# Kernel optimization log

Hardware: AMD Instinct MI355X
Metric: run time of the kernel (lower is better)

The kernel has to match this reference:

```python
import jax, jax.numpy as jnp
import numpy as np

N_NODE = 50000
D_FEAT = 128
N_EDGE = 625000
SIM_THRESH = 0.1


def setup_inputs() -> dict:
    key = jax.random.key(0)
    k1, k2, k3, k4, k5 = jax.random.split(key, 5)
    features = jax.random.normal(k1, (N_NODE, D_FEAT), dtype=jnp.float32)
    edge_weight = jax.random.uniform(k2, (N_EDGE,), dtype=jnp.float32)
    gate = jax.random.uniform(k3, (1,), dtype=jnp.float32)
    row = jax.random.randint(k4, (N_EDGE,), 0, N_NODE)
    col = jax.random.randint(k5, (N_EDGE,), 0, N_NODE)
    # avoid self-loops so the original's att[0,0]==0 / diagonal-removal branches
    # behave as the common (no self-loop) path
    col = jnp.where(col == row, (col + 1) % N_NODE, col)
    edge_index = jnp.stack([row, col], axis=0).astype(jnp.int64)
    return {"edge_index": edge_index, "edge_weight": edge_weight,
            "features": features, "gate": gate}


def reference(edge_index, edge_weight, features, gate):
    n_node = features.shape[0]
    row, col = edge_index[0], edge_index[1]
    # per-edge cosine similarity via normalized feature gather
    nrm = jnp.maximum(jnp.linalg.norm(features, axis=1, keepdims=True), 1e-12)
    fn = features / nrm
    sim = jnp.sum(fn[row] * fn[col], axis=1)            # [E]
    sim = jnp.where(sim < SIM_THRESH, 0.0, sim)         # threshold (all remaining >= 0.1)
    # row-wise L1 normalize over the sparse adjacency
    row_sum = jax.ops.segment_sum(jnp.abs(sim), row, num_segments=n_node)  # [N]
    denom = jnp.where(row_sum > 0, row_sum, 1.0)
    sim_norm = sim / denom[row]
    # degree-based self-loop weight lam = 1/(deg+1); only affects diagonal edges
    degree = jax.ops.segment_sum((sim_norm != 0).astype(sim_norm.dtype), row,
                                 num_segments=n_node)
    lam = 1.0 / (degree + 1.0)
    att_edge = sim_norm + jnp.where(row == col, lam[row], 0.0)
    att_edge = jnp.exp(att_edge)
    # learnable gate blend + clamp
    out = gate[0] * edge_weight + (1.0 - gate[0]) * att_edge
    return jnp.maximum(out, 0.0)
```

## Files before the change

### kernel.cpp

```cpp
#include <hip/hip_runtime.h>
#include <hip/hip_fp16.h>
#include <math.h>

#define N_NODE 50000
#define D_FEAT 128
#define N_EDGE 625000
#define SIM_THRESH 0.1f
#define BAND_EPS 1e-3f


__global__ void prep_kernel(const float* __restrict__ feat,
                            float* __restrict__ inv_nrm,
                            __half* __restrict__ fn16,
                            float* __restrict__ row_sum,
                            float* __restrict__ degree,
                            unsigned int* __restrict__ band_count) {
    int g = blockIdx.x * blockDim.x + threadIdx.x;
    if (g < N_NODE) { row_sum[g] = 0.0f; degree[g] = 0.0f; }
    if (g == 0) *band_count = 0u;
    int node = g >> 5;
    int lane = g & 31;
    if (node >= N_NODE) return;
    const float4* f = (const float4*)(feat + (size_t)node * D_FEAT);
    float4 v = f[lane];
    float ss = v.x * v.x + v.y * v.y + v.z * v.z + v.w * v.w;
#pragma unroll
    for (int o = 16; o > 0; o >>= 1)
        ss += __shfl_down(ss, o, 32);
    ss = __shfl(ss, 0, 32);
    float inv = 1.0f / fmaxf(sqrtf(ss), 1e-12f);
    if (lane == 0) inv_nrm[node] = inv;
    __half2 h0 = __floats2half2_rn(v.x * inv, v.y * inv);
    __half2 h1 = __floats2half2_rn(v.z * inv, v.w * inv);
    __half2* dst = (__half2*)(fn16 + (size_t)node * D_FEAT);
    dst[lane * 2]     = h0;
    dst[lane * 2 + 1] = h1;
}

__global__ void edge_sim16_kernel(const int* __restrict__ row,
                                  const int* __restrict__ col,
                                  const __half* __restrict__ fn16,
                                  float* __restrict__ sim_out,
                                  float* __restrict__ row_sum,
                                  float* __restrict__ degree,
                                  unsigned int* __restrict__ band_count,
                                  unsigned int* __restrict__ band_list) {
    int g = blockIdx.x * blockDim.x + threadIdx.x;
    int edge = g >> 4;
    int lane = g & 15;
    if (edge >= N_EDGE) return;
    int r = row[edge];
    int c = col[edge];
    float4 a = ((const float4*)(fn16 + (size_t)r * D_FEAT))[lane];
    float4 b = ((const float4*)(fn16 + (size_t)c * D_FEAT))[lane];
    const __half2* ah = (const __half2*)&a;
    const __half2* bh = (const __half2*)&b;
    float d = 0.0f;
#pragma unroll
    for (int i = 0; i < 4; i++) {
        float2 af = __half22float2(ah[i]);
        float2 bf = __half22float2(bh[i]);
        d = fmaf(af.x, bf.x, d);
        d = fmaf(af.y, bf.y, d);
    }
#pragma unroll
    for (int o = 8; o > 0; o >>= 1)
        d += __shfl_down(d, o, 16);
    if (lane == 0) {
        float s = d;
        if (fabsf(s - SIM_THRESH) < BAND_EPS) {
            unsigned int idx = atomicAdd(band_count, 1u);
            band_list[idx] = (unsigned int)edge;
        } else {
            if (s < SIM_THRESH) s = 0.0f;
            sim_out[edge] = s;
            if (s != 0.0f) {
                atomicAdd(&row_sum[r], s);
                atomicAdd(&degree[r], 1.0f);
            }
        }
    }
}

__global__ void band_fix_kernel(const int* __restrict__ row,
                                const int* __restrict__ col,
                                const float* __restrict__ feat,
                                const float* __restrict__ inv_nrm,
                                const unsigned int* __restrict__ band_count,
                                const unsigned int* __restrict__ band_list,
                                float* __restrict__ sim_out,
                                float* __restrict__ row_sum,
                                float* __restrict__ degree) {
    int g = blockIdx.x * blockDim.x + threadIdx.x;
    int group = g >> 5;
    int lane = g & 31;
    int ngroups = (gridDim.x * blockDim.x) >> 5;
    unsigned int cnt = *band_count;
    for (unsigned int i = group; i < cnt; i += ngroups) {
        int e = (int)band_list[i];
        int r = row[e], c = col[e];
        float4 a = ((const float4*)(feat + (size_t)r * D_FEAT))[lane];
        float4 b = ((const float4*)(feat + (size_t)c * D_FEAT))[lane];
        float d = a.x * b.x + a.y * b.y + a.z * b.z + a.w * b.w;
#pragma unroll
        for (int o = 16; o > 0; o >>= 1)
            d += __shfl_down(d, o, 32);
        if (lane == 0) {
            float s = d * inv_nrm[r] * inv_nrm[c];
            if (s < SIM_THRESH) s = 0.0f;
            sim_out[e] = s;
            if (s != 0.0f) {
                atomicAdd(&row_sum[r], s);
                atomicAdd(&degree[r], 1.0f);
            }
        }
    }
}

__global__ void edge_out_kernel(const int* __restrict__ row,
                                const int* __restrict__ col,
                                const float* __restrict__ sim,
                                const float* __restrict__ row_sum,
                                const float* __restrict__ degree,
                                const float* __restrict__ ew,
                                const float* __restrict__ gate,
                                float* __restrict__ out) {
    int e = blockIdx.x * blockDim.x + threadIdx.x;
    if (e >= N_EDGE) return;
    int r = row[e];
    float rs = row_sum[r];
    float denom = (rs > 0.0f) ? rs : 1.0f;
    float att = sim[e] / denom;
    if (r == col[e]) att += 1.0f / (degree[r] + 1.0f);
    att = expf(att);
    float gv = gate[0];
    float o = gv * ew[e] + (1.0f - gv) * att;
    out[e] = fmaxf(o, 0.0f);
}

__global__ void inv_norm_kernel(const float* __restrict__ feat,
                                float* __restrict__ inv_nrm) {
    int g = blockIdx.x * blockDim.x + threadIdx.x;
    int node = g >> 5;
    int lane = g & 31;
    if (node >= N_NODE) return;
    const float4* f = (const float4*)(feat + (size_t)node * D_FEAT);
    float4 v = f[lane];
    float ss = v.x * v.x + v.y * v.y + v.z * v.z + v.w * v.w;
#pragma unroll
    for (int o = 16; o > 0; o >>= 1)
        ss += __shfl_down(ss, o, 32);
    if (lane == 0) {
        float n = fmaxf(sqrtf(ss), 1e-12f);
        inv_nrm[node] = 1.0f / n;
    }
}

__global__ void edge_sim_kernel(const int* __restrict__ row,
                                const int* __restrict__ col,
                                const float* __restrict__ feat,
                                const float* __restrict__ inv_nrm,
                                float* __restrict__ sim_out,
                                float* __restrict__ row_sum,
                                float* __restrict__ degree) {
    int g = blockIdx.x * blockDim.x + threadIdx.x;
    int edge = g >> 5;
    int lane = g & 31;
    if (edge >= N_EDGE) return;
    int r = row[edge];
    int c = col[edge];
    float4 a = ((const float4*)(feat + (size_t)r * D_FEAT))[lane];
    float4 b = ((const float4*)(feat + (size_t)c * D_FEAT))[lane];
    float d = a.x * b.x + a.y * b.y + a.z * b.z + a.w * b.w;
#pragma unroll
    for (int o = 16; o > 0; o >>= 1)
        d += __shfl_down(d, o, 32);
    if (lane == 0) {
        float s = d * inv_nrm[r] * inv_nrm[c];
        if (s < SIM_THRESH) s = 0.0f;
        sim_out[edge] = s;
        if (s != 0.0f) {
            atomicAdd(&row_sum[r], s);
            atomicAdd(&degree[r], 1.0f);
        }
    }
}

extern "C" void kernel_launch(void* const* d_in, const int* in_sizes, int n_in,
                              void* d_out, int out_size, void* d_ws, size_t ws_size,
                              hipStream_t stream) {
    const int*   edge_index = (const int*)d_in[0];
    const float* ew         = (const float*)d_in[1];
    const float* feat       = (const float*)d_in[2];
    const float* gate       = (const float*)d_in[3];
    float*       out        = (float*)d_out;

    const int* row = edge_index;
    const int* col = edge_index + N_EDGE;

    float* row_sum = (float*)d_ws;
    float* degree  = row_sum + N_NODE;
    float* inv_nrm = degree + N_NODE;
    float* sim     = inv_nrm + N_NODE;
    __half* fn16   = (__half*)(sim + N_EDGE);
    unsigned int* band_list  = (unsigned int*)(fn16 + (size_t)N_NODE * D_FEAT);
    unsigned int* band_count = band_list + N_EDGE;

    size_t need = (size_t)(3 * N_NODE + N_EDGE) * 4
                + (size_t)N_NODE * D_FEAT * 2
                + (size_t)(N_EDGE + 1) * 4;

    const int block = 256;

    if (ws_size >= need) {
        {
            long long threads = (long long)N_NODE * 32;
            prep_kernel<<<(int)((threads + block - 1) / block), block, 0, stream>>>(
                feat, inv_nrm, fn16, row_sum, degree, band_count);
        }
        {
            long long threads = (long long)N_EDGE * 16;
            edge_sim16_kernel<<<(int)((threads + block - 1) / block), block, 0, stream>>>(
                row, col, fn16, sim, row_sum, degree, band_count, band_list);
        }
        band_fix_kernel<<<64, block, 0, stream>>>(
            row, col, feat, inv_nrm, band_count, band_list, sim, row_sum, degree);
        edge_out_kernel<<<(N_EDGE + block - 1) / block, block, 0, stream>>>(
            row, col, sim, row_sum, degree, ew, gate, out);
    } else {
        hipMemsetAsync(d_ws, 0, (size_t)2 * N_NODE * sizeof(float), stream);
        {
            long long threads = (long long)N_NODE * 32;
            inv_norm_kernel<<<(int)((threads + block - 1) / block), block, 0, stream>>>(
                feat, inv_nrm);
        }
        {
            long long threads = (long long)N_EDGE * 32;
            edge_sim_kernel<<<(int)((threads + block - 1) / block), block, 0, stream>>>(
                row, col, feat, inv_nrm, sim, row_sum, degree);
        }
        edge_out_kernel<<<(N_EDGE + block - 1) / block, block, 0, stream>>>(
            row, col, sim, row_sum, degree, ew, gate, out);
    }
}
```

Baseline: 149.5 us.

## Screen edges with fp8 dot product before fp16 and fp32 refinement

Adds an fp8 copy of the normalized features and computes a cheap fp8 dot product per edge first. Only edges whose fp8 similarity exceeds a screening bound (0.07) load fp16 features, and near-threshold edges fall back inline to fp32, which replaces the separate band list and band-fix kernel. This cuts gather traffic for the many edges far below the threshold and drops one kernel launch. The risk is that fp8 error could wrongly drop edges with true similarity just above 0.1, and the inline fp32 path adds divergence.

```diff
diff --git a/kernel.cpp b/kernel.cpp
--- a/kernel.cpp
+++ b/kernel.cpp
@@ -6,113 +6,112 @@
 #define D_FEAT 128
 #define N_EDGE 625000
 #define SIM_THRESH 0.1f
-#define BAND_EPS 1e-3f
-
+#define SCREEN_LO 0.07f
+#define BAND_EPS 5e-4f
+
+typedef float v2f __attribute__((ext_vector_type(2)));
 
 __global__ void prep_kernel(const float* __restrict__ feat,
                             float* __restrict__ inv_nrm,
                             __half* __restrict__ fn16,
+                            unsigned int* __restrict__ fp8tab,
                             float* __restrict__ row_sum,
-                            float* __restrict__ degree,
-                            unsigned int* __restrict__ band_count) {
+                            float* __restrict__ degree) {
     int g = blockIdx.x * blockDim.x + threadIdx.x;
     if (g < N_NODE) { row_sum[g] = 0.0f; degree[g] = 0.0f; }
-    if (g == 0) *band_count = 0u;
     int node = g >> 5;
     int lane = g & 31;
     if (node >= N_NODE) return;
-    const float4* f = (const float4*)(feat + (size_t)node * D_FEAT);
-    float4 v = f[lane];
+    float4 v = ((const float4*)(feat + (size_t)node * D_FEAT))[lane];
     float ss = v.x * v.x + v.y * v.y + v.z * v.z + v.w * v.w;
 #pragma unroll
-    for (int o = 16; o > 0; o >>= 1)
-        ss += __shfl_down(ss, o, 32);
+    for (int o = 16; o > 0; o >>= 1) ss += __shfl_down(ss, o, 32);
     ss = __shfl(ss, 0, 32);
     float inv = 1.0f / fmaxf(sqrtf(ss), 1e-12f);
     if (lane == 0) inv_nrm[node] = inv;
-    __half2 h0 = __floats2half2_rn(v.x * inv, v.y * inv);
-    __half2 h1 = __floats2half2_rn(v.z * inv, v.w * inv);
-    __half2* dst = (__half2*)(fn16 + (size_t)node * D_FEAT);
-    dst[lane * 2]     = h0;
-    dst[lane * 2 + 1] = h1;
-}
-
-__global__ void edge_sim16_kernel(const int* __restrict__ row,
-                                  const int* __restrict__ col,
-                                  const __half* __restrict__ fn16,
-                                  float* __restrict__ sim_out,
-                                  float* __restrict__ row_sum,
-                                  float* __restrict__ degree,
-                                  unsigned int* __restrict__ band_count,
-                                  unsigned int* __restrict__ band_list) {
+    float x0 = v.x * inv, x1 = v.y * inv, x2 = v.z * inv, x3 = v.w * inv;
+    __half2 h0 = __floats2half2_rn(x0, x1);
+    __half2 h1 = __floats2half2_rn(x2, x3);
+    uint2 p;
+    p.x = *(unsigned int*)&h0;
+    p.y = *(unsigned int*)&h1;
+    ((uint2*)(fn16 + (size_t)node * D_FEAT))[lane] = p;
+    int w = __builtin_amdgcn_cvt_pk_fp8_f32(x0, x1, 0, false);
+    w = __builtin_amdgcn_cvt_pk_fp8_f32(x2, x3, w, true);
+    fp8tab[(size_t)node * 32 + lane] = (unsigned int)w;
+}
+
+__global__ void edge_sim8_kernel(const int* __restrict__ row,
+                                 const int* __restrict__ col,
+                                 const float* __restrict__ feat,
+                                 const float* __restrict__ inv_nrm,
+                                 const __half* __restrict__ fn16,
+                                 const unsigned int* __restrict__ fp8tab,
+                                 float* __restrict__ sim_out,
+                                 float* __restrict__ row_sum,
+                                 float* __restrict__ degree) {
     int g = blockIdx.x * blockDim.x + threadIdx.x;
     int edge = g >> 4;
     int lane = g & 15;
     if (edge >= N_EDGE) return;
     int r = row[edge];
     int c = col[edge];
-    float4 a = ((const float4*)(fn16 + (size_t)r * D_FEAT))[lane];
-    float4 b = ((const float4*)(fn16 + (size_t)c * D_FEAT))[lane];
-    const __half2* ah = (const __half2*)&a;
-    const __half2* bh = (const __half2*)&b;
+
+    uint2 aw = ((const uint2*)(fp8tab + (size_t)r * 32))[lane];
+    uint2 bw = ((const uint2*)(fp8tab + (size_t)c * 32))[lane];
+    v2f a01 = __builtin_amdgcn_cvt_pk_f32_fp8((int)aw.x, false);
+    v2f a23 = __builtin_amdgcn_cvt_pk_f32_fp8((int)aw.x, true);
+    v2f a45 = __builtin_amdgcn_cvt_pk_f32_fp8((int)aw.y, false);
+    v2f a67 = __builtin_amdgcn_cvt_pk_f32_fp8((int)aw.y, true);
+    v2f b01 = __builtin_amdgcn_cvt_pk_f32_fp8((int)bw.x, false);
+    v2f b23 = __builtin_amdgcn_cvt_pk_f32_fp8((int)bw.x, true);
+    v2f b45 = __builtin_amdgcn_cvt_pk_f32_fp8((int)bw.y, false);
+    v2f b67 = __builtin_amdgcn_cvt_pk_f32_fp8((int)bw.y, true);
     float d = 0.0f;
-#pragma unroll
-    for (int i = 0; i < 4; i++) {
-        float2 af = __half22float2(ah[i]);
-        float2 bf = __half22float2(bh[i]);
-        d = fmaf(af.x, bf.x, d);
-        d = fmaf(af.y, bf.y, d);
-    }
-#pragma unroll
-    for (int o = 8; o > 0; o >>= 1)
-        d += __shfl_down(d, o, 16);
+    d = fmaf(a01.x, b01.x, d); d = fmaf(a01.y, b01.y, d);
+    d = fmaf(a23.x, b23.x, d); d = fmaf(a23.y, b23.y, d);
+    d = fmaf(a45.x, b45.x, d); d = fmaf(a45.y, b45.y, d);
+    d = fmaf(a67.x, b67.x, d); d = fmaf(a67.y, b67.y, d);
+#pragma unroll
+    for (int o = 8; o > 0; o >>= 1) d += __shfl_down(d, o, 16);
+    d = __shfl(d, 0, 16);
+
+    float s = 0.0f;
+    if (d > SCREEN_LO) {
+        float4 a = ((const float4*)(fn16 + (size_t)r * D_FEAT))[lane];
+        float4 b = ((const float4*)(fn16 + (size_t)c * D_FEAT))[lane];
+        const __half2* ah = (const __half2*)&a;
+        const __half2* bh = (const __half2*)&b;
+        float dh = 0.0f;
+#pragma unroll
+        for (int i = 0; i < 4; i++) {
+            float2 af = __half22float2(ah[i]);
+            float2 bf = __half22float2(bh[i]);
+            dh = fmaf(af.x, bf.x, dh);
+            dh = fmaf(af.y, bf.y, dh);
+        }
+#pragma unroll
+        for (int o = 8; o > 0; o >>= 1) dh += __shfl_down(dh, o, 16);
+        dh = __shfl(dh, 0, 16);
+        if (fabsf(dh - SIM_THRESH) < BAND_EPS) {
+            const float4* fr = (const float4*)(feat + (size_t)r * D_FEAT);
+            const float4* fc = (const float4*)(feat + (size_t)c * D_FEAT);
+            float4 a0 = fr[lane], a1 = fr[lane + 16];
+            float4 b0 = fc[lane], b1 = fc[lane + 16];
+            float dd = a0.x * b0.x + a0.y * b0.y + a0.z * b0.z + a0.w * b0.w
+                     + a1.x * b1.x + a1.y * b1.y + a1.z * b1.z + a1.w * b1.w;
+#pragma unroll
+            for (int o = 8; o > 0; o >>= 1) dd += __shfl_down(dd, o, 16);
+            dd = __shfl(dd, 0, 16);
+            dh = dd * inv_nrm[r] * inv_nrm[c];
+        }
+        s = (dh < SIM_THRESH) ? 0.0f : dh;
+    }
     if (lane == 0) {
-        float s = d;
-        if (fabsf(s - SIM_THRESH) < BAND_EPS) {
-            unsigned int idx = atomicAdd(band_count, 1u);
-            band_list[idx] = (unsigned int)edge;
-        } else {
-            if (s < SIM_THRESH) s = 0.0f;
-            sim_out[edge] = s;
-            if (s != 0.0f) {
-                atomicAdd(&row_sum[r], s);
-                atomicAdd(&degree[r], 1.0f);
-            }
-        }
-    }
-}
-
-__global__ void band_fix_kernel(const int* __restrict__ row,
-                                const int* __restrict__ col,
-                                const float* __restrict__ feat,
-                                const float* __restrict__ inv_nrm,
-                                const unsigned int* __restrict__ band_count,
-                                const unsigned int* __restrict__ band_list,
-                                float* __restrict__ sim_out,
-                                float* __restrict__ row_sum,
-                                float* __restrict__ degree) {
-    int g = blockIdx.x * blockDim.x + threadIdx.x;
-    int group = g >> 5;
-    int lane = g & 31;
-    int ngroups = (gridDim.x * blockDim.x) >> 5;
-    unsigned int cnt = *band_count;
-    for (unsigned int i = group; i < cnt; i += ngroups) {
-        int e = (int)band_list[i];
-        int r = row[e], c = col[e];
-        float4 a = ((const float4*)(feat + (size_t)r * D_FEAT))[lane];
-        float4 b = ((const float4*)(feat + (size_t)c * D_FEAT))[lane];
-        float d = a.x * b.x + a.y * b.y + a.z * b.z + a.w * b.w;
-#pragma unroll
-        for (int o = 16; o > 0; o >>= 1)
-            d += __shfl_down(d, o, 32);
-        if (lane == 0) {
-            float s = d * inv_nrm[r] * inv_nrm[c];
-            if (s < SIM_THRESH) s = 0.0f;
-            sim_out[e] = s;
-            if (s != 0.0f) {
-                atomicAdd(&row_sum[r], s);
-                atomicAdd(&degree[r], 1.0f);
-            }
+        sim_out[edge] = s;
+        if (s != 0.0f) {
+            atomicAdd(&row_sum[r], s);
+            atomicAdd(&degree[r], 1.0f);
         }
     }
 }
@@ -139,21 +138,19 @@
 }
 
 __global__ void inv_norm_kernel(const float* __restrict__ feat,
-                                float* __restrict__ inv_nrm) {
-    int g = blockIdx.x * blockDim.x + threadIdx.x;
+                                float* __restrict__ inv_nrm,
+                                float* __restrict__ row_sum,
+                                float* __restrict__ degree) {
+    int g = blockIdx.x * blockDim.x + threadIdx.x;
+    if (g < N_NODE) { row_sum[g] = 0.0f; degree[g] = 0.0f; }
     int node = g >> 5;
     int lane = g & 31;
     if (node >= N_NODE) return;
-    const float4* f = (const float4*)(feat + (size_t)node * D_FEAT);
-    float4 v = f[lane];
+    float4 v = ((const float4*)(feat + (size_t)node * D_FEAT))[lane];
     float ss = v.x * v.x + v.y * v.y + v.z * v.z + v.w * v.w;
 #pragma unroll
-    for (int o = 16; o > 0; o >>= 1)
-        ss += __shfl_down(ss, o, 32);
-    if (lane == 0) {
-        float n = fmaxf(sqrtf(ss), 1e-12f);
-        inv_nrm[node] = 1.0f / n;
-    }
+    for (int o = 16; o > 0; o >>= 1) ss += __shfl_down(ss, o, 32);
+    if (lane == 0) inv_nrm[node] = 1.0f / fmaxf(sqrtf(ss), 1e-12f);
 }
 
 __global__ void edge_sim_kernel(const int* __restrict__ row,
@@ -173,8 +170,7 @@
     float4 b = ((const float4*)(feat + (size_t)c * D_FEAT))[lane];
     float d = a.x * b.x + a.y * b.y + a.z * b.z + a.w * b.w;
 #pragma unroll
-    for (int o = 16; o > 0; o >>= 1)
-        d += __shfl_down(d, o, 32);
+    for (int o = 16; o > 0; o >>= 1) d += __shfl_down(d, o, 32);
     if (lane == 0) {
         float s = d * inv_nrm[r] * inv_nrm[c];
         if (s < SIM_THRESH) s = 0.0f;
@@ -203,12 +199,11 @@
     float* inv_nrm = degree + N_NODE;
     float* sim     = inv_nrm + N_NODE;
     __half* fn16   = (__half*)(sim + N_EDGE);
-    unsigned int* band_list  = (unsigned int*)(fn16 + (size_t)N_NODE * D_FEAT);
-    unsigned int* band_count = band_list + N_EDGE;
+    unsigned int* fp8tab = (unsigned int*)(fn16 + (size_t)N_NODE * D_FEAT);
 
     size_t need = (size_t)(3 * N_NODE + N_EDGE) * 4
                 + (size_t)N_NODE * D_FEAT * 2
-                + (size_t)(N_EDGE + 1) * 4;
+                + (size_t)N_NODE * D_FEAT;
 
     const int block = 256;
 
@@ -216,23 +211,20 @@
         {
             long long threads = (long long)N_NODE * 32;
             prep_kernel<<<(int)((threads + block - 1) / block), block, 0, stream>>>(
-                feat, inv_nrm, fn16, row_sum, degree, band_count);
+                feat, inv_nrm, fn16, fp8tab, row_sum, degree);
         }
         {
             long long threads = (long long)N_EDGE * 16;
-            edge_sim16_kernel<<<(int)((threads + block - 1) / block), block, 0, stream>>>(
-                row, col, fn16, sim, row_sum, degree, band_count, band_list);
-        }
-        band_fix_kernel<<<64, block, 0, stream>>>(
-            row, col, feat, inv_nrm, band_count, band_list, sim, row_sum, degree);
+            edge_sim8_kernel<<<(int)((threads + block - 1) / block), block, 0, stream>>>(
+                row, col, feat, inv_nrm, fn16, fp8tab, sim, row_sum, degree);
+        }
         edge_out_kernel<<<(N_EDGE + block - 1) / block, block, 0, stream>>>(
             row, col, sim, row_sum, degree, ew, gate, out);
     } else {
-        hipMemsetAsync(d_ws, 0, (size_t)2 * N_NODE * sizeof(float), stream);
         {
             long long threads = (long long)N_NODE * 32;
             inv_norm_kernel<<<(int)((threads + block - 1) / block), block, 0, stream>>>(
-                feat, inv_nrm);
+                feat, inv_nrm, row_sum, degree);
         }
         {
             long long threads = (long long)N_EDGE * 32;
```

New measurement: 134.6 us. 1.11x faster.
